# Performance work log

Measured on AMD Instinct MI355X. Metric: run time of the kernel, lower is better.

The kernel has to match this reference:

```python
import jax, jax.numpy as jnp
import numpy as np

D_EMB = 1024
D_HEAD = 64
B = 4
T = 4096


def setup_inputs() -> dict:
    key = jax.random.key(0)
    kx, kk, kq, kv = jax.random.split(key, 4)
    s = 1.0 / np.sqrt(D_EMB)  # torch Linear default init scale (uniform bound)
    x = jax.random.normal(kx, (B, T, D_EMB), dtype=jnp.float32)
    Wk = jax.random.uniform(kk, (D_HEAD, D_EMB), jnp.float32, -s, s)
    Wq = jax.random.uniform(kq, (D_HEAD, D_EMB), jnp.float32, -s, s)
    Wv = jax.random.uniform(kv, (D_HEAD, D_EMB), jnp.float32, -s, s)
    return {"x": x, "Wk": Wk, "Wq": Wq, "Wv": Wv}


def reference(x, Wk, Wq, Wv):
    # x: (B, T, d_emb); W*: (d_head, d_emb) -- torch Linear stores (out, in)
    k = jnp.einsum('bte,he->bth', x, Wk)
    q = jnp.einsum('bte,he->bth', x, Wq)
    v = jnp.einsum('bte,he->bth', x, Wv)
    scale = D_HEAD ** (-0.5)
    a = jnp.einsum('bth,bsh->bts', q, k) * scale  # (B, T, T)
    Tlen = x.shape[-2]
    causal = jnp.tril(jnp.ones((Tlen, Tlen), dtype=bool))
    a = jnp.where(causal, a, -jnp.inf)
    a = jax.nn.softmax(a, axis=-1)
    return jnp.einsum('bts,bsh->bth', a, v)  # (B, T, d_head)
```

## Files before the change

kernel.cpp:

```cpp
#include <hip/hip_runtime.h>
#include <hip/hip_bf16.h>

#define D_EMB 1024
#define T_LEN 4096
#define NTASK2 544

typedef short short8 __attribute__((ext_vector_type(8)));
typedef float f32x4 __attribute__((ext_vector_type(4)));
typedef float f32x16 __attribute__((ext_vector_type(16)));
typedef float float4v __attribute__((ext_vector_type(4)));

__device__ __forceinline__ unsigned short f32_to_bf16(float f) {
    union { float f; unsigned int u; } c; c.f = f;
    unsigned int u = c.u;
    return (unsigned short)((u + 0x7FFFu + ((u >> 16) & 1u)) >> 16);
}
__device__ __forceinline__ float bf16_to_f32(unsigned short v) {
    union { unsigned int u; float f; } c; c.u = ((unsigned int)v) << 16;
    return c.f;
}
__device__ __forceinline__ unsigned cvtpk_bf16(float a, float b) {
    unsigned r;
    asm("v_cvt_pk_bf16_f32 %0, %1, %2" : "=v"(r) : "v"(a), "v"(b));
    return r;
}
__device__ __forceinline__ float xhalf_max(float x) {
    return fmaxf(x, __shfl_xor(x, 32));
}
__device__ __forceinline__ float xhalf_add(float x) {
    return x + __shfl_xor(x, 32);
}
__device__ __forceinline__ void gl_lds16(const void* g, void* l) {
    __builtin_amdgcn_global_load_lds(
        (const __attribute__((address_space(1))) unsigned int*)(g),
        (__attribute__((address_space(3))) unsigned int*)(l), 16, 0, 0);
}

#define QSCALE (0.125f * 1.44269504f)

__global__ __launch_bounds__(256) void convert_w(const float* __restrict__ Wk,
                                                 const float* __restrict__ Wq,
                                                 const float* __restrict__ Wv,
                                                 unsigned short* __restrict__ Wb) {
    int e = (blockIdx.x * 256 + threadIdx.x) * 8;
    const float* src;
    if (e < 65536) src = Wk + e;
    else if (e < 131072) src = Wq + (e - 65536);
    else src = Wv + (e - 131072);
    float4v a0 = *(const float4v*)src;
    float4v a1 = *(const float4v*)(src + 4);
    short8 r;
    r[0] = (short)f32_to_bf16(a0[0]); r[1] = (short)f32_to_bf16(a0[1]);
    r[2] = (short)f32_to_bf16(a0[2]); r[3] = (short)f32_to_bf16(a0[3]);
    r[4] = (short)f32_to_bf16(a1[0]); r[5] = (short)f32_to_bf16(a1[1]);
    r[6] = (short)f32_to_bf16(a1[2]); r[7] = (short)f32_to_bf16(a1[3]);
    int row = e >> 10;
    int dst = e ^ ((row & 7) << 3);
    *(short8*)(Wb + dst) = r;
}

__global__ __launch_bounds__(256, 2) void qkv_proj(const float* __restrict__ x,
                                                   const unsigned short* __restrict__ Wb,
                                                   unsigned short* __restrict__ Kb,
                                                   unsigned short* __restrict__ Qb,
                                                   unsigned short* __restrict__ Vt) {
    __shared__ __attribute__((aligned(16))) unsigned short Xl[16 * 1024];
    __shared__ __attribute__((aligned(16))) unsigned short Wsl[2][12288];

    int tid = threadIdx.x;
    int lane = tid & 63, wave = tid >> 6;
    int lo = lane & 15, hi = lane >> 4;
    int row0 = blockIdx.x * 16;

    {
        int r = tid >> 4, ii = tid & 15;
        const float* xrow = x + (size_t)(row0 + r) * D_EMB + ii * 4;
        float4v xv[16];
#pragma unroll
        for (int j = 0; j < 16; j++) xv[j] = *(const float4v*)(xrow + j * 64);
#pragma unroll
        for (int j = 0; j < 6; j++) {
            int unit = j * 4 + wave;
            int u = unit * 64 + lane;
            gl_lds16(Wb + (size_t)(u >> 3) * D_EMB + (u & 7) * 8, &Wsl[0][unit * 512]);
        }
        unsigned swz = (unsigned)((r & 7) << 4);
        char* xl = (char*)Xl + r * 2048;
#pragma unroll
        for (int j = 0; j < 16; j++) {
            unsigned w0 = cvtpk_bf16(xv[j][0], xv[j][1]);
            unsigned w1 = cvtpk_bf16(xv[j][2], xv[j][3]);
            *(uint2*)(xl + (((unsigned)(j * 128 + ii * 8)) ^ swz)) = make_uint2(w0, w1);
        }
    }
    __syncthreads();

    f32x4 acc0 = (f32x4){0.f, 0.f, 0.f, 0.f};
    f32x4 acc1 = (f32x4){0.f, 0.f, 0.f, 0.f};
    f32x4 acc2 = (f32x4){0.f, 0.f, 0.f, 0.f};
    int xorm = (lo & 7) << 4;
    const char* xbase = (const char*)Xl + lo * 2048;
    int rowb = wave * 48 + lo;

    for (int kt = 0; kt < 16; kt++) {
        if (kt < 15) {
            int k0n = (kt + 1) * 64;
#pragma unroll
            for (int j = 0; j < 6; j++) {
                int unit = j * 4 + wave;
                int u = unit * 64 + lane;
                gl_lds16(Wb + (size_t)(u >> 3) * D_EMB + k0n + (u & 7) * 8,
                         &Wsl[(kt + 1) & 1][unit * 512]);
            }
            __builtin_amdgcn_sched_barrier(0);
            asm volatile("s_waitcnt vmcnt(6)" ::: "memory");
        } else {
            __builtin_amdgcn_sched_barrier(0);
            asm volatile("s_waitcnt vmcnt(0)" ::: "memory");
        }
        __builtin_amdgcn_s_barrier();
        __builtin_amdgcn_sched_barrier(0);

        const char* sb = (const char*)&Wsl[kt & 1][0];
#pragma unroll
        for (int ks = 0; ks < 2; ks++) {
            int xoff = (kt * 128 + ks * 64 + hi * 16) ^ xorm;
            short8 af = *(const short8*)(xbase + xoff);
            int boff = (ks * 64 + hi * 16) ^ xorm;
            short8 b0 = *(const short8*)(sb + rowb * 128 + boff);
            short8 b1 = *(const short8*)(sb + (rowb + 16) * 128 + boff);
            short8 b2 = *(const short8*)(sb + (rowb + 32) * 128 + boff);
            acc0 = __builtin_amdgcn_mfma_f32_16x16x32_bf16(af, b0, acc0, 0, 0, 0);
            acc1 = __builtin_amdgcn_mfma_f32_16x16x32_bf16(af, b1, acc1, 0, 0, 0);
            acc2 = __builtin_amdgcn_mfma_f32_16x16x32_bf16(af, b2, acc2, 0, 0, 0);
        }
        asm volatile("s_waitcnt lgkmcnt(0)" ::: "memory");
        __builtin_amdgcn_s_barrier();
        __builtin_amdgcn_sched_barrier(0);
    }

    f32x4 accs[3] = {acc0, acc1, acc2};
#pragma unroll
    for (int i = 0; i < 3; i++) {
        int n = wave * 3 + i;
#pragma unroll
        for (int r = 0; r < 4; r++) {
            int grow = row0 + hi * 4 + r;
            float val = accs[i][r];
            if (n < 4) {
                Kb[(size_t)grow * 64 + n * 16 + lo] = f32_to_bf16(val);
            } else if (n < 8) {
                Qb[(size_t)grow * 64 + (n - 4) * 16 + lo] = f32_to_bf16(val * QSCALE);
            } else {
                int bb = grow >> 12;
                Vt[((size_t)bb * 64 + (n - 8) * 16 + lo) * T_LEN + (grow & 4095)] = f32_to_bf16(val);
            }
        }
    }
}

__global__ __launch_bounds__(64, 3) void attn(const unsigned short* __restrict__ Qb,
                                              const unsigned short* __restrict__ Kb,
                                              const unsigned short* __restrict__ Vt,
                                              unsigned short* __restrict__ Opart,
                                              float* __restrict__ Mpart,
                                              float* __restrict__ Lpart) {
    int lane = threadIdx.x;
    int q32 = lane & 31;
    int hi = lane >> 5;
    unsigned lin = blockIdx.x;
    int b = lin & 3;
    int s = (int)(((lin >> 3) << 1) | ((lin >> 2) & 1));

    int k = 16, rem = s;
    while (rem >= 4 * k) { rem -= 4 * k; k--; }
    int ti = rem / k;
    int st = 4 * k - 1 - ti;
    int c = rem - ti * k;

    int u0 = c * 8;
    int u1 = min(u0 + 8, 2 * st + 2);
    int ta = 2 * st, tb = ta + 1;
    int qrowA = 64 * st + q32;
    int qrowB = qrowA + 32;

    size_t base = (size_t)b * T_LEN;

    short8 qfa[4], qfb[4];
    const unsigned short* qpa = Qb + (base + qrowA) * 64 + hi * 8;
    const unsigned short* qpb = Qb + (base + qrowB) * 64 + hi * 8;
#pragma unroll
    for (int d = 0; d < 4; d++) {
        qfa[d] = *(const short8*)(qpa + d * 16);
        qfb[d] = *(const short8*)(qpb + d * 16);
    }

    size_t vbase = ((size_t)b * 64 + q32) * T_LEN;
    f32x16 oA0 = {0.f}, oA1 = {0.f}, oB0 = {0.f}, oB1 = {0.f};
    float mA = -3e38f, lA = 0.f, mB = -3e38f, lB = 0.f;

    for (int u = u0; u < u1; ++u) {
        const unsigned short* kp = Kb + (base + u * 32 + q32) * 64 + hi * 8;
        short8 kc0 = *(const short8*)kp;
        short8 kc1 = *(const short8*)(kp + 16);
        short8 kc2 = *(const short8*)(kp + 32);
        short8 kc3 = *(const short8*)(kp + 48);
        const unsigned short* vp = Vt + vbase + u * 32 + hi * 8;
        short8 vc0 = *(const short8*)vp;
        short8 vc1 = *(const short8*)(vp + 16);
        short8 vc2 = *(const short8*)(vp + 32 * T_LEN);
        short8 vc3 = *(const short8*)(vp + 32 * T_LEN + 16);

        f32x16 sa = {0.f}, sb = {0.f};
        sa = __builtin_amdgcn_mfma_f32_32x32x16_bf16(kc0, qfa[0], sa, 0, 0, 0);
        sb = __builtin_amdgcn_mfma_f32_32x32x16_bf16(kc0, qfb[0], sb, 0, 0, 0);
        sa = __builtin_amdgcn_mfma_f32_32x32x16_bf16(kc1, qfa[1], sa, 0, 0, 0);
        sb = __builtin_amdgcn_mfma_f32_32x32x16_bf16(kc1, qfb[1], sb, 0, 0, 0);
        sa = __builtin_amdgcn_mfma_f32_32x32x16_bf16(kc2, qfa[2], sa, 0, 0, 0);
        sb = __builtin_amdgcn_mfma_f32_32x32x16_bf16(kc2, qfb[2], sb, 0, 0, 0);
        sa = __builtin_amdgcn_mfma_f32_32x32x16_bf16(kc3, qfa[3], sa, 0, 0, 0);
        sb = __builtin_amdgcn_mfma_f32_32x32x16_bf16(kc3, qfb[3], sb, 0, 0, 0);

        if (u >= ta) {
#pragma unroll
            for (int r = 0; r < 16; ++r) {
                int key = 32 * u + (r & 3) + 8 * (r >> 2) + 4 * hi;
                sa[r] = (key <= qrowA) ? sa[r] : -3e38f;
                if (u == tb) sb[r] = (key <= qrowB) ? sb[r] : -3e38f;
            }
        }

        float a0 = fmaxf(fmaxf(sa[0], sa[1]), sa[2]);
        float a1 = fmaxf(fmaxf(sa[3], sa[4]), sa[5]);
        float a2 = fmaxf(fmaxf(sa[6], sa[7]), sa[8]);
        float a3 = fmaxf(fmaxf(sa[9], sa[10]), sa[11]);
        float a4 = fmaxf(fmaxf(sa[12], sa[13]), sa[14]);
        float mxA = fmaxf(fmaxf(fmaxf(a0, a1), fmaxf(a2, a3)), fmaxf(a4, sa[15]));
        float b0 = fmaxf(fmaxf(sb[0], sb[1]), sb[2]);
        float b1 = fmaxf(fmaxf(sb[3], sb[4]), sb[5]);
        float b2 = fmaxf(fmaxf(sb[6], sb[7]), sb[8]);
        float b3 = fmaxf(fmaxf(sb[9], sb[10]), sb[11]);
        float b4 = fmaxf(fmaxf(sb[12], sb[13]), sb[14]);
        float mxB = fmaxf(fmaxf(fmaxf(b0, b1), fmaxf(b2, b3)), fmaxf(b4, sb[15]));
        mxA = xhalf_max(mxA);
        mxB = xhalf_max(mxB);

        float grow = fmaxf(mxA - mA, mxB - mB);
        if (__any(grow > 8.0f)) {
            float mnA = fmaxf(mA, mxA);
            float alA = exp2f(mA - mnA);
            mA = mnA; lA *= alA;
            float mnB = fmaxf(mB, mxB);
            float alB = exp2f(mB - mnB);
            mB = mnB; lB *= alB;
#pragma unroll
            for (int r = 0; r < 16; ++r) {
                oA0[r] *= alA; oA1[r] *= alA;
                oB0[r] *= alB; oB1[r] *= alB;
            }
        }

#pragma unroll
        for (int r = 0; r < 16; ++r) {
            sa[r] = exp2f(sa[r] - mA);
            sb[r] = exp2f(sb[r] - mB);
        }
        float yA = ((sa[0] + sa[8]) + (sa[4] + sa[12])) + ((sa[1] + sa[9]) + (sa[5] + sa[13]))
                 + ((sa[2] + sa[10]) + (sa[6] + sa[14])) + ((sa[3] + sa[11]) + (sa[7] + sa[15]));
        float yB = ((sb[0] + sb[8]) + (sb[4] + sb[12])) + ((sb[1] + sb[9]) + (sb[5] + sb[13]))
                 + ((sb[2] + sb[10]) + (sb[6] + sb[14])) + ((sb[3] + sb[11]) + (sb[7] + sb[15]));
        lA += xhalf_add(yA);
        lB += xhalf_add(yB);

        unsigned pa0 = cvtpk_bf16(sa[0],  sa[1]);
        unsigned pa1 = cvtpk_bf16(sa[2],  sa[3]);
        unsigned pa2 = cvtpk_bf16(sa[4],  sa[5]);
        unsigned pa3 = cvtpk_bf16(sa[6],  sa[7]);
        unsigned pa4 = cvtpk_bf16(sa[8],  sa[9]);
        unsigned pa5 = cvtpk_bf16(sa[10], sa[11]);
        unsigned pa6 = cvtpk_bf16(sa[12], sa[13]);
        unsigned pa7 = cvtpk_bf16(sa[14], sa[15]);
        unsigned pb0 = cvtpk_bf16(sb[0],  sb[1]);
        unsigned pb1 = cvtpk_bf16(sb[2],  sb[3]);
        unsigned pb2 = cvtpk_bf16(sb[4],  sb[5]);
        unsigned pb3 = cvtpk_bf16(sb[6],  sb[7]);
        unsigned pb4 = cvtpk_bf16(sb[8],  sb[9]);
        unsigned pb5 = cvtpk_bf16(sb[10], sb[11]);
        unsigned pb6 = cvtpk_bf16(sb[12], sb[13]);
        unsigned pb7 = cvtpk_bf16(sb[14], sb[15]);
        asm("v_permlane32_swap_b32 %0, %1" : "+v"(pa0), "+v"(pa2));
        asm("v_permlane32_swap_b32 %0, %1" : "+v"(pa1), "+v"(pa3));
        asm("v_permlane32_swap_b32 %0, %1" : "+v"(pa4), "+v"(pa6));
        asm("v_permlane32_swap_b32 %0, %1" : "+v"(pa5), "+v"(pa7));
        asm("v_permlane32_swap_b32 %0, %1" : "+v"(pb0), "+v"(pb2));
        asm("v_permlane32_swap_b32 %0, %1" : "+v"(pb1), "+v"(pb3));
        asm("v_permlane32_swap_b32 %0, %1" : "+v"(pb4), "+v"(pb6));
        asm("v_permlane32_swap_b32 %0, %1" : "+v"(pb5), "+v"(pb7));
        union U8 { unsigned u[4]; short8 s; };
        U8 fA0; fA0.u[0] = pa0; fA0.u[1] = pa1; fA0.u[2] = pa2; fA0.u[3] = pa3;
        U8 fA1; fA1.u[0] = pa4; fA1.u[1] = pa5; fA1.u[2] = pa6; fA1.u[3] = pa7;
        U8 fB0; fB0.u[0] = pb0; fB0.u[1] = pb1; fB0.u[2] = pb2; fB0.u[3] = pb3;
        U8 fB1; fB1.u[0] = pb4; fB1.u[1] = pb5; fB1.u[2] = pb6; fB1.u[3] = pb7;

        oA0 = __builtin_amdgcn_mfma_f32_32x32x16_bf16(vc0, fA0.s, oA0, 0, 0, 0);
        oB0 = __builtin_amdgcn_mfma_f32_32x32x16_bf16(vc0, fB0.s, oB0, 0, 0, 0);
        oA0 = __builtin_amdgcn_mfma_f32_32x32x16_bf16(vc1, fA1.s, oA0, 0, 0, 0);
        oB0 = __builtin_amdgcn_mfma_f32_32x32x16_bf16(vc1, fB1.s, oB0, 0, 0, 0);
        oA1 = __builtin_amdgcn_mfma_f32_32x32x16_bf16(vc2, fA0.s, oA1, 0, 0, 0);
        oB1 = __builtin_amdgcn_mfma_f32_32x32x16_bf16(vc2, fB0.s, oB1, 0, 0, 0);
        oA1 = __builtin_amdgcn_mfma_f32_32x32x16_bf16(vc3, fA1.s, oA1, 0, 0, 0);
        oB1 = __builtin_amdgcn_mfma_f32_32x32x16_bf16(vc3, fB1.s, oB1, 0, 0, 0);
    }

    int slotA = (b * NTASK2 + s) * 2;
    size_t tbA = ((size_t)slotA * 32 + q32) * 64;
    size_t tbB = ((size_t)(slotA + 1) * 32 + q32) * 64;
#pragma unroll
    for (int hb = 0; hb < 2; hb++) {
#pragma unroll
        for (int g = 0; g < 4; g++) {
            float eA0 = hb ? oA1[4 * g] : oA0[4 * g];
            float eA1 = hb ? oA1[4 * g + 1] : oA0[4 * g + 1];
            float eA2 = hb ? oA1[4 * g + 2] : oA0[4 * g + 2];
            float eA3 = hb ? oA1[4 * g + 3] : oA0[4 * g + 3];
            float eB0 = hb ? oB1[4 * g] : oB0[4 * g];
            float eB1 = hb ? oB1[4 * g + 1] : oB0[4 * g + 1];
            float eB2 = hb ? oB1[4 * g + 2] : oB0[4 * g + 2];
            float eB3 = hb ? oB1[4 * g + 3] : oB0[4 * g + 3];
            int h0 = hb * 32 + g * 8 + hi * 4;
            *reinterpret_cast<uint2*>(Opart + tbA + h0) =
                make_uint2(cvtpk_bf16(eA0, eA1), cvtpk_bf16(eA2, eA3));
            *reinterpret_cast<uint2*>(Opart + tbB + h0) =
                make_uint2(cvtpk_bf16(eB0, eB1), cvtpk_bf16(eB2, eB3));
        }
    }
    if (lane < 32) {
        Mpart[slotA * 32 + q32] = mA;
        Lpart[slotA * 32 + q32] = lA;
        Mpart[(slotA + 1) * 32 + q32] = mB;
        Lpart[(slotA + 1) * 32 + q32] = lB;
    }
}

__global__ __launch_bounds__(256) void attn_merge(const unsigned short* __restrict__ Opart,
                                                  const float* __restrict__ Mpart,
                                                  const float* __restrict__ Lpart,
                                                  float* __restrict__ out) {
    int tid = threadIdx.x;
    int g = blockIdx.x * 64 + (tid >> 2);
    int h0 = (tid & 3) * 16;
    int b = g >> 12, t = g & 4095;
    int tile32 = t >> 5, r32 = t & 31;
    int st = tile32 >> 1, member = tile32 & 1;
    int k = (st >> 2) + 1;
    int sbase = 4 * (136 - ((k * (k + 1)) >> 1));
    int ti = 4 * k - 1 - st;
    int s0 = sbase + ti * k;
    int slot0 = (b * NTASK2 + s0) * 2 + member;

    float mm = -3e38f;
    for (int i = 0; i < k; i++) mm = fmaxf(mm, Mpart[(slot0 + 2 * i) * 32 + r32]);
    float ll = 0.f;
    float acc[16];
#pragma unroll
    for (int e = 0; e < 16; e++) acc[e] = 0.f;
    for (int i = 0; i < k; i++) {
        int slot = slot0 + 2 * i;
        float a = exp2f(Mpart[slot * 32 + r32] - mm);
        ll += a * Lpart[slot * 32 + r32];
        const unsigned short* op = Opart + ((size_t)slot * 32 + r32) * 64 + h0;
        short8 v0 = *(const short8*)op;
        short8 v1 = *(const short8*)(op + 8);
#pragma unroll
        for (int e = 0; e < 8; e++) {
            acc[e]     += a * bf16_to_f32((unsigned short)v0[e]);
            acc[8 + e] += a * bf16_to_f32((unsigned short)v1[e]);
        }
    }
    float inv = 1.f / ll;
    float* dst = out + (size_t)g * 64 + h0;
#pragma unroll
    for (int e = 0; e < 16; e++) dst[e] = acc[e] * inv;
}

extern "C" void kernel_launch(void* const* d_in, const int* in_sizes, int n_in,
                              void* d_out, int out_size, void* d_ws, size_t ws_size,
                              hipStream_t stream) {
    (void)in_sizes; (void)n_in; (void)out_size; (void)ws_size;
    const float* x  = (const float*)d_in[0];
    const float* Wk = (const float*)d_in[1];
    const float* Wq = (const float*)d_in[2];
    const float* Wv = (const float*)d_in[3];
    float* out = (float*)d_out;

    unsigned short* Wb = (unsigned short*)d_ws;
    unsigned short* Kb = Wb + 196608;
    unsigned short* Qb = Kb + 1048576;
    unsigned short* Vt = Qb + 1048576;
    unsigned short* Opart = Vt + 1048576;
    float* Mpart = (float*)(Opart + (size_t)4 * NTASK2 * 2 * 32 * 64);
    float* Lpart = Mpart + 4 * NTASK2 * 2 * 32;

    hipLaunchKernelGGL(convert_w, dim3(96), dim3(256), 0, stream, Wk, Wq, Wv, Wb);
    hipLaunchKernelGGL(qkv_proj, dim3(1024), dim3(256), 0, stream, x, Wb, Kb, Qb, Vt);
    hipLaunchKernelGGL(attn, dim3(4 * NTASK2), dim3(64), 0, stream, Qb, Kb, Vt, Opart, Mpart, Lpart);
    hipLaunchKernelGGL(attn_merge, dim3(256), dim3(256), 0, stream, Opart, Mpart, Lpart, out);
}
```

Before: 84.18 us.

## Pre-tile weights into MFMA fragment order and deepen QKV projection pipeline to four stages

```diff
diff --git a/kernel.cpp b/kernel.cpp
--- a/kernel.cpp
+++ b/kernel.cpp
@@ -41,49 +41,56 @@
 __global__ __launch_bounds__(256) void convert_w(const float* __restrict__ Wk,
                                                  const float* __restrict__ Wq,
                                                  const float* __restrict__ Wv,
-                                                 unsigned short* __restrict__ Wb) {
-    int e = (blockIdx.x * 256 + threadIdx.x) * 8;
+                                                 unsigned short* __restrict__ Wb2) {
+    int i = blockIdx.x * 256 + threadIdx.x;
+    int r = i >> 7;
+    int o = (i & 127) * 8;
     const float* src;
-    if (e < 65536) src = Wk + e;
-    else if (e < 131072) src = Wq + (e - 65536);
-    else src = Wv + (e - 131072);
+    if (r < 64) src = Wk + (size_t)r * D_EMB + o;
+    else if (r < 128) src = Wq + (size_t)(r - 64) * D_EMB + o;
+    else src = Wv + (size_t)(r - 128) * D_EMB + o;
     float4v a0 = *(const float4v*)src;
     float4v a1 = *(const float4v*)(src + 4);
-    short8 r;
-    r[0] = (short)f32_to_bf16(a0[0]); r[1] = (short)f32_to_bf16(a0[1]);
-    r[2] = (short)f32_to_bf16(a0[2]); r[3] = (short)f32_to_bf16(a0[3]);
-    r[4] = (short)f32_to_bf16(a1[0]); r[5] = (short)f32_to_bf16(a1[1]);
-    r[6] = (short)f32_to_bf16(a1[2]); r[7] = (short)f32_to_bf16(a1[3]);
-    int row = e >> 10;
-    int dst = e ^ ((row & 7) << 3);
-    *(short8*)(Wb + dst) = r;
+    short8 v;
+    v[0] = (short)f32_to_bf16(a0[0]); v[1] = (short)f32_to_bf16(a0[1]);
+    v[2] = (short)f32_to_bf16(a0[2]); v[3] = (short)f32_to_bf16(a0[3]);
+    v[4] = (short)f32_to_bf16(a1[0]); v[5] = (short)f32_to_bf16(a1[1]);
+    v[6] = (short)f32_to_bf16(a1[2]); v[7] = (short)f32_to_bf16(a1[3]);
+    int kt = o >> 5;
+    int sc = (o >> 3) & 3;
+    int oc = (kt * 4 + sc) * 192 + r;
+    *(short8*)(Wb2 + (size_t)oc * 8) = v;
 }
 
 __global__ __launch_bounds__(256, 2) void qkv_proj(const float* __restrict__ x,
-                                                   const unsigned short* __restrict__ Wb,
+                                                   const unsigned short* __restrict__ Wb2,
                                                    unsigned short* __restrict__ Kb,
                                                    unsigned short* __restrict__ Qb,
                                                    unsigned short* __restrict__ Vt) {
     __shared__ __attribute__((aligned(16))) unsigned short Xl[16 * 1024];
-    __shared__ __attribute__((aligned(16))) unsigned short Wsl[2][12288];
+    __shared__ __attribute__((aligned(16))) unsigned short Wsl[4][6144];
 
     int tid = threadIdx.x;
     int lane = tid & 63, wave = tid >> 6;
     int lo = lane & 15, hi = lane >> 4;
     int row0 = blockIdx.x * 16;
 
+#pragma unroll
+    for (int kt0 = 0; kt0 < 3; kt0++) {
+#pragma unroll
+        for (int j = 0; j < 3; j++) {
+            int unit = j * 4 + wave;
+            int u = unit * 64 + lane;
+            gl_lds16(Wb2 + ((size_t)kt0 * 768 + u) * 8, &Wsl[kt0][unit * 512]);
+        }
+    }
+
     {
         int r = tid >> 4, ii = tid & 15;
         const float* xrow = x + (size_t)(row0 + r) * D_EMB + ii * 4;
         float4v xv[16];
 #pragma unroll
         for (int j = 0; j < 16; j++) xv[j] = *(const float4v*)(xrow + j * 64);
-#pragma unroll
-        for (int j = 0; j < 6; j++) {
-            int unit = j * 4 + wave;
-            int u = unit * 64 + lane;
-            gl_lds16(Wb + (size_t)(u >> 3) * D_EMB + (u & 7) * 8, &Wsl[0][unit * 512]);
-        }
         unsigned swz = (unsigned)((r & 7) << 4);
         char* xl = (char*)Xl + r * 2048;
 #pragma unroll
@@ -100,43 +107,34 @@
     f32x4 acc2 = (f32x4){0.f, 0.f, 0.f, 0.f};
     int xorm = (lo & 7) << 4;
     const char* xbase = (const char*)Xl + lo * 2048;
-    int rowb = wave * 48 + lo;
-
-    for (int kt = 0; kt < 16; kt++) {
-        if (kt < 15) {
-            int k0n = (kt + 1) * 64;
-#pragma unroll
-            for (int j = 0; j < 6; j++) {
+    int wb_off = hi * 3072 + (wave * 48 + lo) * 16;
+
+    for (int kt = 0; kt < 32; kt++) {
+        __builtin_amdgcn_s_barrier();
+        if (kt + 3 < 32) {
+            int ktn = kt + 3;
+#pragma unroll
+            for (int j = 0; j < 3; j++) {
                 int unit = j * 4 + wave;
                 int u = unit * 64 + lane;
-                gl_lds16(Wb + (size_t)(u >> 3) * D_EMB + k0n + (u & 7) * 8,
-                         &Wsl[(kt + 1) & 1][unit * 512]);
+                gl_lds16(Wb2 + ((size_t)ktn * 768 + u) * 8, &Wsl[ktn & 3][unit * 512]);
             }
-            __builtin_amdgcn_sched_barrier(0);
-            asm volatile("s_waitcnt vmcnt(6)" ::: "memory");
-        } else {
-            __builtin_amdgcn_sched_barrier(0);
-            asm volatile("s_waitcnt vmcnt(0)" ::: "memory");
-        }
-        __builtin_amdgcn_s_barrier();
+        }
         __builtin_amdgcn_sched_barrier(0);
-
-        const char* sb = (const char*)&Wsl[kt & 1][0];
-#pragma unroll
-        for (int ks = 0; ks < 2; ks++) {
-            int xoff = (kt * 128 + ks * 64 + hi * 16) ^ xorm;
-            short8 af = *(const short8*)(xbase + xoff);
-            int boff = (ks * 64 + hi * 16) ^ xorm;
-            short8 b0 = *(const short8*)(sb + rowb * 128 + boff);
-            short8 b1 = *(const short8*)(sb + (rowb + 16) * 128 + boff);
-            short8 b2 = *(const short8*)(sb + (rowb + 32) * 128 + boff);
-            acc0 = __builtin_amdgcn_mfma_f32_16x16x32_bf16(af, b0, acc0, 0, 0, 0);
-            acc1 = __builtin_amdgcn_mfma_f32_16x16x32_bf16(af, b1, acc1, 0, 0, 0);
-            acc2 = __builtin_amdgcn_mfma_f32_16x16x32_bf16(af, b2, acc2, 0, 0, 0);
-        }
-        asm volatile("s_waitcnt lgkmcnt(0)" ::: "memory");
-        __builtin_amdgcn_s_barrier();
+        if (kt < 29)      asm volatile("s_waitcnt vmcnt(9)" ::: "memory");
+        else if (kt == 29) asm volatile("s_waitcnt vmcnt(6)" ::: "memory");
+        else if (kt == 30) asm volatile("s_waitcnt vmcnt(3)" ::: "memory");
+        else               asm volatile("s_waitcnt vmcnt(0)" ::: "memory");
         __builtin_amdgcn_sched_barrier(0);
+
+        short8 af = *(const short8*)(xbase + ((kt * 64 + hi * 16) ^ xorm));
+        const char* wb = (const char*)&Wsl[kt & 3][0] + wb_off;
+        short8 b0 = *(const short8*)(wb);
+        short8 b1 = *(const short8*)(wb + 256);
+        short8 b2 = *(const short8*)(wb + 512);
+        acc0 = __builtin_amdgcn_mfma_f32_16x16x32_bf16(af, b0, acc0, 0, 0, 0);
+        acc1 = __builtin_amdgcn_mfma_f32_16x16x32_bf16(af, b1, acc1, 0, 0, 0);
+        acc2 = __builtin_amdgcn_mfma_f32_16x16x32_bf16(af, b2, acc2, 0, 0, 0);
     }
 
     f32x4 accs[3] = {acc0, acc1, acc2};
@@ -393,16 +391,16 @@
     const float* Wv = (const float*)d_in[3];
     float* out = (float*)d_out;
 
-    unsigned short* Wb = (unsigned short*)d_ws;
-    unsigned short* Kb = Wb + 196608;
+    unsigned short* Wb2 = (unsigned short*)d_ws;
+    unsigned short* Kb = Wb2 + 196608;
     unsigned short* Qb = Kb + 1048576;
     unsigned short* Vt = Qb + 1048576;
     unsigned short* Opart = Vt + 1048576;
     float* Mpart = (float*)(Opart + (size_t)4 * NTASK2 * 2 * 32 * 64);
     float* Lpart = Mpart + 4 * NTASK2 * 2 * 32;
 
-    hipLaunchKernelGGL(convert_w, dim3(96), dim3(256), 0, stream, Wk, Wq, Wv, Wb);
-    hipLaunchKernelGGL(qkv_proj, dim3(1024), dim3(256), 0, stream, x, Wb, Kb, Qb, Vt);
+    hipLaunchKernelGGL(convert_w, dim3(96), dim3(256), 0, stream, Wk, Wq, Wv, Wb2);
+    hipLaunchKernelGGL(qkv_proj, dim3(1024), dim3(256), 0, stream, x, Wb2, Kb, Qb, Vt);
     hipLaunchKernelGGL(attn, dim3(4 * NTASK2), dim3(64), 0, stream, Qb, Kb, Vt, Opart, Mpart, Lpart);
     hipLaunchKernelGGL(attn_merge, dim3(256), dim3(256), 0, stream, Opart, Mpart, Lpart, out);
 }
```

New measurement: 95.53 us. 13.5% more time.
